# Kernel optimization log

Hardware: AMD Instinct MI355X
Metric: run time of the kernel (lower is better)

## Reference

```python
import jax, jax.numpy as jnp
import numpy as np
import math

D, NH, DFF = 1024, 16, 4096
B, S = 2, 2048
EPS = 1e-5


def _mha(q_in, k_in, v_in, wq, bq, wk, bk, wv, bv, wo, bo, mask):
    Bq, Sq, Dm = q_in.shape
    Sk = k_in.shape[1]
    dh = Dm // NH
    q = (q_in @ wq + bq).reshape(Bq, Sq, NH, dh).transpose(0, 2, 1, 3)
    k = (k_in @ wk + bk).reshape(Bq, Sk, NH, dh).transpose(0, 2, 1, 3)
    v = (v_in @ wv + bv).reshape(Bq, Sk, NH, dh).transpose(0, 2, 1, 3)
    scores = jnp.einsum('bhqd,bhkd->bhqk', q, k) / math.sqrt(dh)
    scores = jnp.where(mask == 0, jnp.float32(-1e9), scores)
    w = jax.nn.softmax(scores, axis=-1)
    out = jnp.einsum('bhqk,bhkd->bhqd', w, v)
    out = out.transpose(0, 2, 1, 3).reshape(Bq, Sq, Dm)
    return out @ wo + bo


def _ln(x, g, b):
    mu = jnp.mean(x, axis=-1, keepdims=True)
    var = jnp.var(x, axis=-1, keepdims=True)
    return (x - mu) * jax.lax.rsqrt(var + EPS) * g + b


def setup_inputs() -> dict:
    key = jax.random.key(0)
    ks = jax.random.split(key, 20)
    sc = 1.0 / math.sqrt(D)
    inp = {
        'x': jax.random.normal(ks[0], (B, S, D), jnp.float32),
        'encoder_output': jax.random.normal(ks[1], (B, S, D), jnp.float32),
        'src_mask': jnp.ones((B, 1, 1, S), jnp.int32),
        'tgt_mask': jnp.tril(jnp.ones((S, S), jnp.int32))[None, None],
    }
    names = ['s_wq', 's_wk', 's_wv', 's_wo', 'c_wq', 'c_wk', 'c_wv', 'c_wo']
    for i, n in enumerate(names):
        inp[n] = jax.random.normal(ks[2 + i], (D, D), jnp.float32) * sc
        inp[n.replace('w', 'b')] = jnp.zeros((D,), jnp.float32)
    inp['ff_w1'] = jax.random.normal(ks[10], (D, DFF), jnp.float32) * sc
    inp['ff_b1'] = jnp.zeros((DFF,), jnp.float32)
    inp['ff_w2'] = jax.random.normal(ks[11], (DFF, D), jnp.float32) / math.sqrt(DFF)
    inp['ff_b2'] = jnp.zeros((D,), jnp.float32)
    for i in (1, 2, 3):
        inp[f'ln{i}_g'] = jnp.ones((D,), jnp.float32)
        inp[f'ln{i}_b'] = jnp.zeros((D,), jnp.float32)
    return inp


def reference(x, encoder_output, src_mask, tgt_mask,
              s_wq, s_bq, s_wk, s_bk, s_wv, s_bv, s_wo, s_bo,
              c_wq, c_bq, c_wk, c_bk, c_wv, c_bv, c_wo, c_bo,
              ff_w1, ff_b1, ff_w2, ff_b2,
              ln1_g, ln1_b, ln2_g, ln2_b, ln3_g, ln3_b):
    # self-attention + residual + LN (dropout is identity in eval)
    a = _mha(x, x, x, s_wq, s_bq, s_wk, s_bk, s_wv, s_bv, s_wo, s_bo, tgt_mask)
    x = _ln(x + a, ln1_g, ln1_b)
    # cross-attention
    a = _mha(x, encoder_output, encoder_output,
             c_wq, c_bq, c_wk, c_bk, c_wv, c_bv, c_wo, c_bo, src_mask)
    x = _ln(x + a, ln2_g, ln2_b)
    # FFN
    f = jax.nn.relu(x @ ff_w1 + ff_b1) @ ff_w2 + ff_b2
    return _ln(x + f, ln3_g, ln3_b)
```

## Files before the change

kernel.cpp:

```cpp
#include <hip/hip_runtime.h>
#include <hip/hip_bf16.h>
#include <stdint.h>


#define DEV static __device__ __forceinline__

typedef short bf16s;
typedef __attribute__((ext_vector_type(8))) short bf16x8;
typedef __attribute__((ext_vector_type(4))) float f32x4;

DEV short f2b(float f) {
    union { __hip_bfloat16 h; short s; } u;
    u.h = __float2bfloat16(f);
    return u.s;
}

DEV unsigned pk2(float lo, float hi) {
    union { __hip_bfloat162 h; unsigned u; } u;
    u.h = __float22bfloat162_rn(float2{lo, hi});
    return u.u;
}

DEV f32x4 mfma16(bf16x8 a, bf16x8 b, f32x4 c) {
    return __builtin_amdgcn_mfma_f32_16x16x32_bf16(a, b, c, 0, 0, 0);
}

DEV void gload_lds16(const bf16s* g, short* l) {
    __builtin_amdgcn_global_load_lds(
        (const __attribute__((address_space(1))) void*)g,
        (__attribute__((address_space(3))) void*)l,
        16, 0, 0);
}

__global__ __launch_bounds__(256) void cast2_f32_bf16_kernel(
    const float* __restrict__ a, const float* __restrict__ b,
    bf16s* __restrict__ out, int n)
{
    int i = (blockIdx.x * 256 + threadIdx.x) * 8;
    const float* src = (i < n) ? a : b;
    int j = (i < n) ? i : i - n;
    const float4 u = *(const float4*)(src + j);
    const float4 v = *(const float4*)(src + j + 4);
    bf16x8 r;
    r[0] = f2b(u.x); r[1] = f2b(u.y); r[2] = f2b(u.z); r[3] = f2b(u.w);
    r[4] = f2b(v.x); r[5] = f2b(v.y); r[6] = f2b(v.z); r[7] = f2b(v.w);
    *(bf16x8*)(out + i) = r;
}

struct P8 { const float* p[8]; };

__global__ __launch_bounds__(256) void transpose_cast8_kernel(
    P8 srcs, bf16s* __restrict__ dst)
{
    __shared__ short tile[64][65];
    const float* W = srcs.p[blockIdx.z];
    bf16s* Wt = dst + (size_t)blockIdx.z * 1024 * 1024;
    const int n0 = blockIdx.x * 64, k0 = blockIdx.y * 64;
    const int t = threadIdx.x;
#pragma unroll
    for (int it = 0; it < 16; ++it) {
        int idx = it * 256 + t;
        int r = idx >> 6, c = idx & 63;
        tile[r][c] = f2b(W[(size_t)(k0 + r) * 1024 + n0 + c]);
    }
    __syncthreads();
#pragma unroll
    for (int it = 0; it < 16; ++it) {
        int idx = it * 256 + t;
        int r = idx >> 6, c = idx & 63;
        Wt[(size_t)(n0 + r) * 1024 + k0 + c] = tile[c][r];
    }
}

__global__ __launch_bounds__(256) void transpose_cast_kernel(
    const float* __restrict__ W, bf16s* __restrict__ Wt, int Krows, int Ncols)
{
    __shared__ short tile[64][65];
    const int n0 = blockIdx.x * 64, k0 = blockIdx.y * 64;
    const int t = threadIdx.x;
#pragma unroll
    for (int it = 0; it < 16; ++it) {
        int idx = it * 256 + t;
        int r = idx >> 6, c = idx & 63;
        tile[r][c] = f2b(W[(size_t)(k0 + r) * Ncols + n0 + c]);
    }
    __syncthreads();
#pragma unroll
    for (int it = 0; it < 16; ++it) {
        int idx = it * 256 + t;
        int r = idx >> 6, c = idx & 63;
        Wt[(size_t)(n0 + r) * Krows + k0 + c] = tile[c][r];
    }
}

__global__ __launch_bounds__(256) void transpose_v_kernel(
    const bf16s* __restrict__ V, int ldv, bf16s* __restrict__ Vt, int Sk)
{
    __shared__ short tile[64][65];
    const int s0 = blockIdx.x * 64;
    const int bh = blockIdx.y, b = bh >> 4, h = bh & 15;
    const int t = threadIdx.x;
#pragma unroll
    for (int it = 0; it < 16; ++it) {
        int idx = it * 256 + t;
        int r = idx >> 6, c = idx & 63;
        tile[r][c] = V[(size_t)(b * Sk + s0 + r) * ldv + h * 64 + c];
    }
    __syncthreads();
#pragma unroll
    for (int it = 0; it < 16; ++it) {
        int idx = it * 256 + t;
        int r = idx >> 6, c = idx & 63;
        Vt[((size_t)bh * 64 + r) * Sk + s0 + c] = tile[c][r];
    }
}

__global__ void concat3_kernel(const float* a, const float* b, const float* c,
                               float* o, int n)
{
    int i = blockIdx.x * 256 + threadIdx.x;
    if (i < n) { o[i] = a[i]; o[n + i] = b[i]; o[2 * n + i] = c[i]; }
}
__global__ void concat2_kernel(const float* a, const float* b, float* o, int n)
{
    int i = blockIdx.x * 256 + threadIdx.x;
    if (i < n) { o[i] = a[i]; o[n + i] = b[i]; }
}

template<int BM, int BK, int OUT_BF16, int RELU>
__global__ __launch_bounds__(256, (BM == 64 ? 4 : 2))
void gemm_bt_kernel(const bf16s* __restrict__ A, const bf16s* __restrict__ Bt,
                    const float* __restrict__ bias, void* __restrict__ Cp,
                    int M, int N, int K)
{
    constexpr int BN = 128;
    constexpr int WR = BM / 64;
    constexpr int WC = 4 / WR;
    constexpr int TN = BN / WC;
    constexpr int NF = TN / 16;
    constexpr int NSUB = BK / 32;
    constexpr int RA = BM / 64;
    constexpr int ASUB = BM * 32;
    constexpr int BSUB = BN * 32;
    constexpr int ASZ = NSUB * ASUB;
    constexpr int BSZ = NSUB * BSUB;

    __shared__ short As[2 * ASZ];
    __shared__ short Bs[2 * BSZ];

    const int t = threadIdx.x, lane = t & 63, wave = t >> 6;
    const int g = lane >> 4, ln16 = lane & 15;
    const int wr = wave / WC, wc = wave % WC;
    const int rowA0 = blockIdx.y * BM, rowB0 = blockIdx.x * BN;

    const bf16s* Ab = A + (size_t)rowA0 * K;
    const bf16s* Bb = Bt + (size_t)rowB0 * K;

    f32x4 acc[4][NF] = {};

    auto stage = [&](int buf, int k0) {
        short* Ad = As + buf * ASZ;
        short* Bd = Bs + buf * BSZ;
#pragma unroll
        for (int s = 0; s < NSUB; ++s) {
#pragma unroll
            for (int rnd = 0; rnd < RA; ++rnd) {
                int p = rnd * 256 + t;
                int sr = p >> 3, c3 = (p & 7) ^ (sr & 7);
                int r = sr * 2 + (c3 >> 2), c = c3 & 3;
                gload_lds16(Ab + (size_t)r * K + k0 + s * 32 + c * 8,
                            Ad + s * ASUB + (rnd * 256 + wave * 64) * 8);
            }
#pragma unroll
            for (int rnd = 0; rnd < 2; ++rnd) {
                int p = rnd * 256 + t;
                int sr = p >> 3, c3 = (p & 7) ^ (sr & 7);
                int r = sr * 2 + (c3 >> 2), c = c3 & 3;
                gload_lds16(Bb + (size_t)r * K + k0 + s * 32 + c * 8,
                            Bd + s * BSUB + (rnd * 256 + wave * 64) * 8);
            }
        }
    };

    stage(0, 0);
    __syncthreads();
    int cur = 0;
    for (int k0 = 0; k0 < K; k0 += BK) {
        if (k0 + BK < K) stage(cur ^ 1, k0 + BK);
        const short* Ar0 = As + cur * ASZ;
        const short* Br0 = Bs + cur * BSZ;
#pragma unroll
        for (int s = 0; s < NSUB; ++s) {
            const short* Ar = Ar0 + s * ASUB;
            const short* Br = Br0 + s * BSUB;
            bf16x8 af[4], bfr[NF];
#pragma unroll
            for (int m = 0; m < 4; ++m) {
                int r = wr * 64 + m * 16 + ln16;
                int sr = r >> 1, c3 = (r & 1) * 4 + g;
                af[m] = *(const bf16x8*)(Ar + sr * 64 + ((c3 ^ (sr & 7)) * 8));
            }
#pragma unroll
            for (int n = 0; n < NF; ++n) {
                int r = wc * TN + n * 16 + ln16;
                int sr = r >> 1, c3 = (r & 1) * 4 + g;
                bfr[n] = *(const bf16x8*)(Br + sr * 64 + ((c3 ^ (sr & 7)) * 8));
            }
#pragma unroll
            for (int m = 0; m < 4; ++m)
#pragma unroll
                for (int n = 0; n < NF; ++n)
                    acc[m][n] = mfma16(af[m], bfr[n], acc[m][n]);
        }
        __syncthreads();
        cur ^= 1;
    }

    const int row0 = rowA0 + wr * 64, col0 = rowB0 + wc * TN;
#pragma unroll
    for (int n = 0; n < NF; ++n) {
        const int col = col0 + n * 16 + ln16;
        const float bv = bias[col];
#pragma unroll
        for (int m = 0; m < 4; ++m) {
#pragma unroll
            for (int r = 0; r < 4; ++r) {
                int row = row0 + m * 16 + g * 4 + r;
                float v = acc[m][n][r] + bv;
                if (RELU) v = fmaxf(v, 0.f);
                if (OUT_BF16) ((bf16s*)Cp)[(size_t)row * N + col] = f2b(v);
                else          ((float*)Cp)[(size_t)row * N + col] = v;
            }
        }
    }
}

template<int CAUSAL>
__global__ __launch_bounds__(256, 4)
void flash_kernel(const bf16s* __restrict__ Q, int ldq,
                  const bf16s* __restrict__ K, int ldk,
                  const bf16s* __restrict__ Vt,
                  bf16s* __restrict__ O, int ldo,
                  int Sq, int Sk, float scale)
{
    __shared__ short Ks[2 * 64 * 64];
    __shared__ short Vs[2 * 64 * 64];
    __shared__ short Ps[4 * 16 * 64];
    const int t = threadIdx.x, lane = t & 63, wave = t >> 6;
    const int g = lane >> 4, ln16 = lane & 15;

    const int nqt = Sq >> 6;
    const int id = blockIdx.x;
    const int perx = gridDim.x >> 3;
    const int bhPerX = perx / nqt;
    const int idx = id >> 3;
    const int bh = (id & 7) * bhPerX + idx / nqt;
    int qt = idx % nqt;
    if (CAUSAL) qt = nqt - 1 - qt;
    const int b = bh >> 4, h = bh & 15;
    const int q0 = qt * 64;
    const float sc2 = scale * 1.44269504f;
    const float thrRaw = 8.0f / sc2;

    bf16x8 aq[2];
    {
        const size_t qrow = (size_t)(b * Sq + q0 + wave * 16 + ln16);
#pragma unroll
        for (int kk = 0; kk < 2; ++kk)
            aq[kk] = *(const bf16x8*)(Q + qrow * ldq + h * 64 + kk * 32 + g * 8);
    }

    float m_raw = -1e30f, l_sum = 0.f;
    f32x4 oa[4] = {};

    const int nkt = CAUSAL ? (qt + 1) : (Sk >> 6);
    const bf16s* Kbase = K + (size_t)b * Sk * ldk + h * 64;
    const bf16s* Vbase = Vt + (size_t)bh * 64 * Sk;
    short* myP = Ps + wave * 1024;

    auto stage = [&](int buf, int kt) {
        const bf16s* ksrc = Kbase + (size_t)(kt * 64) * ldk;
        const bf16s* vsrc = Vbase + kt * 64;
        short* Kd = Ks + buf * 4096;
        short* Vd = Vs + buf * 4096;
#pragma unroll
        for (int rnd = 0; rnd < 2; ++rnd) {
            int p = rnd * 256 + t;
            int r = p >> 3, c = (p & 7) ^ (r & 7);
            gload_lds16(ksrc + (size_t)r * ldk + c * 8,
                        Kd + (rnd * 256 + wave * 64) * 8);
        }
#pragma unroll
        for (int rnd = 0; rnd < 2; ++rnd) {
            int p = rnd * 256 + t;
            int r = p >> 3, c = (p & 7) ^ (r & 7);
            gload_lds16(vsrc + (size_t)r * Sk + c * 8,
                        Vd + (rnd * 256 + wave * 64) * 8);
        }
    };

    stage(0, 0);
    __syncthreads();
    int cur = 0;

    for (int kt = 0; kt < nkt; ++kt) {
        if (kt + 1 < nkt) stage(cur ^ 1, kt + 1);
        const short* Kr = Ks + cur * 4096;
        const short* Vr = Vs + cur * 4096;

        f32x4 sa[4] = {};
        __builtin_amdgcn_s_setprio(1);
#pragma unroll
        for (int kk = 0; kk < 2; ++kk) {
#pragma unroll
            for (int n = 0; n < 4; ++n) {
                int key = n * 16 + ln16;
                bf16x8 ak = *(const bf16x8*)(Kr + key * 64 +
                                             (((kk * 4 + g) ^ (key & 7)) * 8));
                sa[n] = mfma16(ak, aq[kk], sa[n]);
            }
        }
        __builtin_amdgcn_s_setprio(0);

        float sv[4][4];
        const bool diag = CAUSAL && (kt == qt);
#pragma unroll
        for (int n = 0; n < 4; ++n)
#pragma unroll
            for (int r = 0; r < 4; ++r) {
                float s = sa[n][r];
                if (diag && (n * 16 + g * 4 + r > wave * 16 + ln16)) s = -1e30f;
                sv[n][r] = s;
            }

        float rm = fmaxf(
            fmaxf(fmaxf(fmaxf(sv[0][0], sv[0][1]), fmaxf(sv[0][2], sv[0][3])),
                  fmaxf(fmaxf(sv[1][0], sv[1][1]), fmaxf(sv[1][2], sv[1][3]))),
            fmaxf(fmaxf(fmaxf(sv[2][0], sv[2][1]), fmaxf(sv[2][2], sv[2][3])),
                  fmaxf(fmaxf(sv[3][0], sv[3][1]), fmaxf(sv[3][2], sv[3][3]))));
        rm = fmaxf(rm, __shfl_xor(rm, 16, 64));
        rm = fmaxf(rm, __shfl_xor(rm, 32, 64));

        if (!__all(rm <= m_raw + thrRaw)) {
            const float mnew = fmaxf(m_raw, rm);
            const float al = exp2f((m_raw - mnew) * sc2);
            m_raw = mnew;
            l_sum *= al;
            float alr[4];
#pragma unroll
            for (int r = 0; r < 4; ++r)
                alr[r] = __shfl(al, g * 4 + r, 64);
#pragma unroll
            for (int n = 0; n < 4; ++n)
#pragma unroll
                for (int r = 0; r < 4; ++r)
                    oa[n][r] *= alr[r];
        }
        const float nm = -m_raw * sc2;

        float rs = 0.f;
#pragma unroll
        for (int n = 0; n < 4; ++n)
#pragma unroll
            for (int r = 0; r < 4; ++r) {
                float p = exp2f(fmaf(sv[n][r], sc2, nm));
                sv[n][r] = p;
                rs += p;
            }
        rs += __shfl_xor(rs, 16, 64);
        rs += __shfl_xor(rs, 32, 64);
        l_sum += rs;

#pragma unroll
        for (int n = 0; n < 4; ++n) {
            uint2 w;
            w.x = pk2(sv[n][0], sv[n][1]);
            w.y = pk2(sv[n][2], sv[n][3]);
            int c = n * 2 + (g >> 1);
            int sh = ln16 * 64 + ((c ^ (ln16 & 7)) * 8) +
                     (((g & 1) ^ (ln16 >> 3)) * 4);
            *(uint2*)(myP + sh) = w;
        }
        asm volatile("s_waitcnt lgkmcnt(0)" ::: "memory");

        __builtin_amdgcn_s_setprio(1);
#pragma unroll
        for (int kk = 0; kk < 2; ++kk) {
            const int base = ln16 * 64 + (((kk * 4 + g) ^ (ln16 & 7)) * 8);
            const int x0 = (ln16 >> 3) * 4;
            union { bf16x8 v; uint2 u2[2]; } pu;
            pu.u2[0] = *(const uint2*)(myP + base + x0);
            pu.u2[1] = *(const uint2*)(myP + base + (x0 ^ 4));
            bf16x8 pa = pu.v;
#pragma unroll
            for (int n = 0; n < 4; ++n) {
                int d = n * 16 + ln16;
                bf16x8 vb = *(const bf16x8*)(Vr + d * 64 +
                                             (((kk * 4 + g) ^ (d & 7)) * 8));
                oa[n] = mfma16(pa, vb, oa[n]);
            }
        }
        __builtin_amdgcn_s_setprio(0);
        __syncthreads();
        cur ^= 1;
    }

    const float inv = 1.f / l_sum;
    float invr[4];
#pragma unroll
    for (int r = 0; r < 4; ++r)
        invr[r] = __shfl(inv, g * 4 + r, 64);
#pragma unroll
    for (int n = 0; n < 4; ++n)
#pragma unroll
        for (int r = 0; r < 4; ++r) {
            int q = q0 + wave * 16 + g * 4 + r;
            int d = h * 64 + n * 16 + ln16;
            O[(size_t)(b * Sq + q) * ldo + d] = f2b(oa[n][r] * invr[r]);
        }
}

template<int WRITE_BF16>
__global__ __launch_bounds__(256)
void add_ln_kernel(const float* __restrict__ X, const float* __restrict__ A,
                   const float* __restrict__ G, const float* __restrict__ Bb,
                   float* __restrict__ Y, bf16s* __restrict__ Yb)
{
    const int row = blockIdx.x, t = threadIdx.x;
    const int lane = t & 63, w = t >> 6;
    const size_t base = (size_t)row * 1024 + t * 4;
    const float4 xv = *(const float4*)(X + base);
    const float4 av = *(const float4*)(A + base);
    float4 v;
    v.x = xv.x + av.x; v.y = xv.y + av.y; v.z = xv.z + av.z; v.w = xv.w + av.w;
    float s = v.x + v.y + v.z + v.w;
    float q = v.x * v.x + v.y * v.y + v.z * v.z + v.w * v.w;
#pragma unroll
    for (int x = 1; x < 64; x <<= 1) {
        s += __shfl_xor(s, x, 64);
        q += __shfl_xor(q, x, 64);
    }
    __shared__ float red[8];
    if (lane == 0) { red[w] = s; red[4 + w] = q; }
    __syncthreads();
    s = red[0] + red[1] + red[2] + red[3];
    q = red[4] + red[5] + red[6] + red[7];
    const float mu = s * (1.f / 1024.f);
    const float var = q * (1.f / 1024.f) - mu * mu;
    const float rstd = rsqrtf(var + 1e-5f);
    const float4 gv = *(const float4*)(G + t * 4);
    const float4 bv = *(const float4*)(Bb + t * 4);
    float o0 = (v.x - mu) * rstd * gv.x + bv.x;
    float o1 = (v.y - mu) * rstd * gv.y + bv.y;
    float o2 = (v.z - mu) * rstd * gv.z + bv.z;
    float o3 = (v.w - mu) * rstd * gv.w + bv.w;
    float4 ov; ov.x = o0; ov.y = o1; ov.z = o2; ov.w = o3;
    *(float4*)(Y + base) = ov;
    if (WRITE_BF16) {
        short4 yb;
        yb.x = f2b(o0); yb.y = f2b(o1); yb.z = f2b(o2); yb.w = f2b(o3);
        *(short4*)(Yb + base) = yb;
    }
}

extern "C" void kernel_launch(void* const* d_in, const int* in_sizes, int n_in,
                              void* d_out, int out_size, void* d_ws, size_t ws_size,
                              hipStream_t stream)
{
    constexpr int Dm = 1024, DFF = 4096, Bq = 2, S = 2048;
    constexpr int NT = Bq * S;
    constexpr size_t MM = (size_t)Dm * Dm;

    const float* x    = (const float*)d_in[0];
    const float* enc  = (const float*)d_in[1];
    const float* s_wq = (const float*)d_in[4];  const float* s_bq = (const float*)d_in[5];
    const float* s_wk = (const float*)d_in[6];  const float* s_bk = (const float*)d_in[7];
    const float* s_wv = (const float*)d_in[8];  const float* s_bv = (const float*)d_in[9];
    const float* s_wo = (const float*)d_in[10]; const float* s_bo = (const float*)d_in[11];
    const float* c_wq = (const float*)d_in[12]; const float* c_bq = (const float*)d_in[13];
    const float* c_wk = (const float*)d_in[14]; const float* c_bk = (const float*)d_in[15];
    const float* c_wv = (const float*)d_in[16]; const float* c_bv = (const float*)d_in[17];
    const float* c_wo = (const float*)d_in[18]; const float* c_bo = (const float*)d_in[19];
    const float* ffw1 = (const float*)d_in[20]; const float* ffb1 = (const float*)d_in[21];
    const float* ffw2 = (const float*)d_in[22]; const float* ffb2 = (const float*)d_in[23];
    const float* ln1g = (const float*)d_in[24]; const float* ln1b = (const float*)d_in[25];
    const float* ln2g = (const float*)d_in[26]; const float* ln2b = (const float*)d_in[27];
    const float* ln3g = (const float*)d_in[28]; const float* ln3b = (const float*)d_in[29];

    char* ws = (char*)d_ws;
    size_t off = 0;
    auto alloc = [&](size_t bytes) -> char* {
        char* p = ws + off;
        off += (bytes + 255) & ~(size_t)255;
        return p;
    };

    bf16s* xbf   = (bf16s*)alloc((size_t)NT * Dm * 2);
    bf16s* encbf = (bf16s*)alloc((size_t)NT * Dm * 2);
    bf16s* wAll  = (bf16s*)alloc(8 * MM * 2);
    bf16s* w1T   = (bf16s*)alloc((size_t)Dm * DFF * 2);
    bf16s* w2T   = (bf16s*)alloc((size_t)Dm * DFF * 2);
    float* bqkv  = (float*)alloc((size_t)3 * Dm * 4);
    float* bkvc  = (float*)alloc((size_t)2 * Dm * 4);
    bf16s* QKV   = (bf16s*)alloc((size_t)NT * 3 * Dm * 2);
    bf16s* Vt    = (bf16s*)alloc((size_t)NT * Dm * 2);
    bf16s* AO    = (bf16s*)alloc((size_t)NT * Dm * 2);
    float* Pbuf  = (float*)alloc((size_t)NT * Dm * 4);
    float* x1f   = (float*)alloc((size_t)NT * Dm * 4);
    bf16s* x1bf  = (bf16s*)alloc((size_t)NT * Dm * 2);
    float* x2f   = (float*)alloc((size_t)NT * Dm * 4);
    bf16s* x2bf  = (bf16s*)alloc((size_t)NT * Dm * 2);
    bf16s* Hbuf  = (bf16s*)alloc((size_t)NT * DFF * 2);
    (void)ws_size; (void)in_sizes; (void)n_in; (void)out_size;

    bf16s* wqkvT = wAll;
    bf16s* woTs  = wAll + 3 * MM;
    bf16s* wqTc  = wAll + 4 * MM;
    bf16s* wkvTc = wAll + 5 * MM;
    bf16s* woTc  = wAll + 7 * MM;

    cast2_f32_bf16_kernel<<<2 * NT * Dm / 8 / 256, 256, 0, stream>>>(
        x, enc, xbf, NT * Dm);
    P8 srcs = {{s_wq, s_wk, s_wv, s_wo, c_wq, c_wk, c_wv, c_wo}};
    transpose_cast8_kernel<<<dim3(16, 16, 8), 256, 0, stream>>>(srcs, wAll);
    transpose_cast_kernel<<<dim3(64, 16), 256, 0, stream>>>(ffw1, w1T, Dm, DFF);
    transpose_cast_kernel<<<dim3(16, 64), 256, 0, stream>>>(ffw2, w2T, DFF, Dm);
    concat3_kernel<<<4, 256, 0, stream>>>(s_bq, s_bk, s_bv, bqkv, Dm);
    concat2_kernel<<<4, 256, 0, stream>>>(c_bk, c_bv, bkvc, Dm);

    gemm_bt_kernel<128, 64, 1, 0><<<dim3(24, 32), 256, 0, stream>>>(
        xbf, wqkvT, bqkv, QKV, NT, 3 * Dm, Dm);
    transpose_v_kernel<<<dim3(32, 32), 256, 0, stream>>>(
        QKV + 2 * Dm, 3 * Dm, Vt, S);
    flash_kernel<1><<<dim3(1024), 256, 0, stream>>>(
        QKV, 3 * Dm, QKV + Dm, 3 * Dm, Vt, AO, Dm, S, S, 0.125f);
    gemm_bt_kernel<64, 32, 0, 0><<<dim3(8, 64), 256, 0, stream>>>(
        AO, woTs, s_bo, Pbuf, NT, Dm, Dm);
    add_ln_kernel<1><<<NT, 256, 0, stream>>>(x, Pbuf, ln1g, ln1b, x1f, x1bf);

    bf16s* Q2  = QKV;
    bf16s* KV2 = QKV + (size_t)NT * Dm;
    gemm_bt_kernel<64, 32, 1, 0><<<dim3(8, 64), 256, 0, stream>>>(
        x1bf, wqTc, c_bq, Q2, NT, Dm, Dm);
    gemm_bt_kernel<128, 64, 1, 0><<<dim3(16, 32), 256, 0, stream>>>(
        encbf, wkvTc, bkvc, KV2, NT, 2 * Dm, Dm);
    transpose_v_kernel<<<dim3(32, 32), 256, 0, stream>>>(
        KV2 + Dm, 2 * Dm, Vt, S);
    flash_kernel<0><<<dim3(1024), 256, 0, stream>>>(
        Q2, Dm, KV2, 2 * Dm, Vt, AO, Dm, S, S, 0.125f);
    gemm_bt_kernel<64, 32, 0, 0><<<dim3(8, 64), 256, 0, stream>>>(
        AO, woTc, c_bo, Pbuf, NT, Dm, Dm);
    add_ln_kernel<1><<<NT, 256, 0, stream>>>(x1f, Pbuf, ln2g, ln2b, x2f, x2bf);

    gemm_bt_kernel<128, 64, 1, 1><<<dim3(32, 32), 256, 0, stream>>>(
        x2bf, w1T, ffb1, Hbuf, NT, DFF, Dm);
    gemm_bt_kernel<64, 32, 0, 0><<<dim3(8, 64), 256, 0, stream>>>(
        Hbuf, w2T, ffb2, Pbuf, NT, Dm, DFF);
    add_ln_kernel<0><<<NT, 256, 0, stream>>>(
        x2f, Pbuf, ln3g, ln3b, (float*)d_out, nullptr);
}
```

Baseline: 606.8 us.

## Interleave causal q-tile order and hoist flash-attention address math

Changes the causal q-tile assignment to alternate heavy and light tiles for better load balance across workgroups. Precomputes swizzled LDS offsets and staging offsets outside the key loop, advancing global pointers incrementally. Replaces exp2f with the raw hardware exp2 builtin and restructures the row-max reduction. The hardware exp2 builtin drops special-case handling, and precomputing the offsets raises register pressure.

```diff
diff --git a/kernel.cpp b/kernel.cpp
--- a/kernel.cpp
+++ b/kernel.cpp
@@ -255,8 +255,8 @@
     const int bhPerX = perx / nqt;
     const int idx = id >> 3;
     const int bh = (id & 7) * bhPerX + idx / nqt;
-    int qt = idx % nqt;
-    if (CAUSAL) qt = nqt - 1 - qt;
+    const int j = idx % nqt;
+    const int qt = CAUSAL ? ((j & 1) ? (j >> 1) : (nqt - 1 - (j >> 1))) : j;
     const int b = bh >> 4, h = bh & 15;
     const int q0 = qt * 64;
     const float sc2 = scale * 1.44269504f;
@@ -270,56 +270,75 @@
             aq[kk] = *(const bf16x8*)(Q + qrow * ldq + h * 64 + kk * 32 + g * 8);
     }
 
+    int qvOff[2][4];
+    int paOff[2];
+    int pWr[4];
+#pragma unroll
+    for (int kk = 0; kk < 2; ++kk) {
+        paOff[kk] = ln16 * 64 + (((kk * 4 + g) ^ (ln16 & 7)) * 8);
+#pragma unroll
+        for (int n = 0; n < 4; ++n) {
+            int key = n * 16 + ln16;
+            qvOff[kk][n] = key * 64 + (((kk * 4 + g) ^ (key & 7)) * 8);
+        }
+    }
+#pragma unroll
+    for (int n = 0; n < 4; ++n) {
+        int c = n * 2 + (g >> 1);
+        pWr[n] = ln16 * 64 + ((c ^ (ln16 & 7)) * 8) +
+                 (((g & 1) ^ (ln16 >> 3)) * 4);
+    }
+    const int x0 = (ln16 >> 3) * 4;
+
+    int sgOffK[2], sgOffV[2], sgLds[2];
+#pragma unroll
+    for (int rnd = 0; rnd < 2; ++rnd) {
+        int p = rnd * 256 + t;
+        int r = p >> 3, c = (p & 7) ^ (r & 7);
+        sgOffK[rnd] = r * ldk + c * 8;
+        sgOffV[rnd] = r * Sk + c * 8;
+        sgLds[rnd]  = (rnd * 256 + wave * 64) * 8;
+    }
+
     float m_raw = -1e30f, l_sum = 0.f;
     f32x4 oa[4] = {};
 
     const int nkt = CAUSAL ? (qt + 1) : (Sk >> 6);
-    const bf16s* Kbase = K + (size_t)b * Sk * ldk + h * 64;
-    const bf16s* Vbase = Vt + (size_t)bh * 64 * Sk;
+    const bf16s* kcur = K + (size_t)b * Sk * ldk + h * 64;
+    const bf16s* vcur = Vt + (size_t)bh * 64 * Sk;
     short* myP = Ps + wave * 1024;
 
-    auto stage = [&](int buf, int kt) {
-        const bf16s* ksrc = Kbase + (size_t)(kt * 64) * ldk;
-        const bf16s* vsrc = Vbase + kt * 64;
-        short* Kd = Ks + buf * 4096;
-        short* Vd = Vs + buf * 4096;
-#pragma unroll
-        for (int rnd = 0; rnd < 2; ++rnd) {
-            int p = rnd * 256 + t;
-            int r = p >> 3, c = (p & 7) ^ (r & 7);
-            gload_lds16(ksrc + (size_t)r * ldk + c * 8,
-                        Kd + (rnd * 256 + wave * 64) * 8);
-        }
-#pragma unroll
-        for (int rnd = 0; rnd < 2; ++rnd) {
-            int p = rnd * 256 + t;
-            int r = p >> 3, c = (p & 7) ^ (r & 7);
-            gload_lds16(vsrc + (size_t)r * Sk + c * 8,
-                        Vd + (rnd * 256 + wave * 64) * 8);
-        }
+    auto stage = [&](int buf) {
+        short* Kd = Ks + (buf << 12);
+        short* Vd = Vs + (buf << 12);
+#pragma unroll
+        for (int rnd = 0; rnd < 2; ++rnd)
+            gload_lds16(kcur + sgOffK[rnd], Kd + sgLds[rnd]);
+#pragma unroll
+        for (int rnd = 0; rnd < 2; ++rnd)
+            gload_lds16(vcur + sgOffV[rnd], Vd + sgLds[rnd]);
     };
 
-    stage(0, 0);
+    stage(0);
+    kcur += (size_t)64 * ldk; vcur += 64;
     __syncthreads();
     int cur = 0;
 
     for (int kt = 0; kt < nkt; ++kt) {
-        if (kt + 1 < nkt) stage(cur ^ 1, kt + 1);
-        const short* Kr = Ks + cur * 4096;
-        const short* Vr = Vs + cur * 4096;
+        if (kt + 1 < nkt) {
+            stage(cur ^ 1);
+            kcur += (size_t)64 * ldk; vcur += 64;
+        }
+        const short* Kr = Ks + (cur << 12);
+        const short* Vr = Vs + (cur << 12);
 
         f32x4 sa[4] = {};
         __builtin_amdgcn_s_setprio(1);
 #pragma unroll
-        for (int kk = 0; kk < 2; ++kk) {
-#pragma unroll
-            for (int n = 0; n < 4; ++n) {
-                int key = n * 16 + ln16;
-                bf16x8 ak = *(const bf16x8*)(Kr + key * 64 +
-                                             (((kk * 4 + g) ^ (key & 7)) * 8));
-                sa[n] = mfma16(ak, aq[kk], sa[n]);
-            }
-        }
+        for (int kk = 0; kk < 2; ++kk)
+#pragma unroll
+            for (int n = 0; n < 4; ++n)
+                sa[n] = mfma16(*(const bf16x8*)(Kr + qvOff[kk][n]), aq[kk], sa[n]);
         __builtin_amdgcn_s_setprio(0);
 
         float sv[4][4];
@@ -333,17 +352,20 @@
                 sv[n][r] = s;
             }
 
-        float rm = fmaxf(
-            fmaxf(fmaxf(fmaxf(sv[0][0], sv[0][1]), fmaxf(sv[0][2], sv[0][3])),
-                  fmaxf(fmaxf(sv[1][0], sv[1][1]), fmaxf(sv[1][2], sv[1][3]))),
-            fmaxf(fmaxf(fmaxf(sv[2][0], sv[2][1]), fmaxf(sv[2][2], sv[2][3])),
-                  fmaxf(fmaxf(sv[3][0], sv[3][1]), fmaxf(sv[3][2], sv[3][3]))));
+        float rm = fmaxf(fmaxf(sv[0][0], sv[0][1]), sv[0][2]);
+        rm = fmaxf(fmaxf(rm, sv[0][3]), sv[1][0]);
+        rm = fmaxf(fmaxf(rm, sv[1][1]), sv[1][2]);
+        rm = fmaxf(fmaxf(rm, sv[1][3]), sv[2][0]);
+        rm = fmaxf(fmaxf(rm, sv[2][1]), sv[2][2]);
+        rm = fmaxf(fmaxf(rm, sv[2][3]), sv[3][0]);
+        rm = fmaxf(fmaxf(rm, sv[3][1]), sv[3][2]);
+        rm = fmaxf(rm, sv[3][3]);
         rm = fmaxf(rm, __shfl_xor(rm, 16, 64));
         rm = fmaxf(rm, __shfl_xor(rm, 32, 64));
 
         if (!__all(rm <= m_raw + thrRaw)) {
             const float mnew = fmaxf(m_raw, rm);
-            const float al = exp2f((m_raw - mnew) * sc2);
+            const float al = __builtin_amdgcn_exp2f((m_raw - mnew) * sc2);
             m_raw = mnew;
             l_sum *= al;
             float alr[4];
@@ -363,7 +385,7 @@
         for (int n = 0; n < 4; ++n)
 #pragma unroll
             for (int r = 0; r < 4; ++r) {
-                float p = exp2f(fmaf(sv[n][r], sc2, nm));
+                float p = __builtin_amdgcn_exp2f(fmaf(sv[n][r], sc2, nm));
                 sv[n][r] = p;
                 rs += p;
             }
@@ -376,29 +398,20 @@
             uint2 w;
             w.x = pk2(sv[n][0], sv[n][1]);
             w.y = pk2(sv[n][2], sv[n][3]);
-            int c = n * 2 + (g >> 1);
-            int sh = ln16 * 64 + ((c ^ (ln16 & 7)) * 8) +
-                     (((g & 1) ^ (ln16 >> 3)) * 4);
-            *(uint2*)(myP + sh) = w;
+            *(uint2*)(myP + pWr[n]) = w;
         }
         asm volatile("s_waitcnt lgkmcnt(0)" ::: "memory");
 
         __builtin_amdgcn_s_setprio(1);
 #pragma unroll
         for (int kk = 0; kk < 2; ++kk) {
-            const int base = ln16 * 64 + (((kk * 4 + g) ^ (ln16 & 7)) * 8);
-            const int x0 = (ln16 >> 3) * 4;
             union { bf16x8 v; uint2 u2[2]; } pu;
-            pu.u2[0] = *(const uint2*)(myP + base + x0);
-            pu.u2[1] = *(const uint2*)(myP + base + (x0 ^ 4));
+            pu.u2[0] = *(const uint2*)(myP + paOff[kk] + x0);
+            pu.u2[1] = *(const uint2*)(myP + paOff[kk] + (x0 ^ 4));
             bf16x8 pa = pu.v;
 #pragma unroll
-            for (int n = 0; n < 4; ++n) {
-                int d = n * 16 + ln16;
-                bf16x8 vb = *(const bf16x8*)(Vr + d * 64 +
-                                             (((kk * 4 + g) ^ (d & 7)) * 8));
-                oa[n] = mfma16(pa, vb, oa[n]);
-            }
+            for (int n = 0; n < 4; ++n)
+                oa[n] = mfma16(pa, *(const bf16x8*)(Vr + qvOff[kk][n]), oa[n]);
         }
         __builtin_amdgcn_s_setprio(0);
         __syncthreads();
```

Result: faster. 576.9 us (-4.9%).
